# Kernel tuning notes

Measured on AMD Instinct MI355X. Metric: run time of the kernel, lower is better.

The kernel has to match this reference:

```python
import jax, jax.numpy as jnp
import numpy as np

D_MODEL = 1024
N_HEADS = 16
HEAD_DIM = D_MODEL // N_HEADS


def setup_inputs() -> dict:
    key = jax.random.key(0)
    k_x, k_wqkv, k_bqkv, k_wo, k_bo = jax.random.split(key, 5)
    B, T = 2, 2048
    scale = 1.0 / np.sqrt(D_MODEL)
    return {
        "x": jax.random.normal(k_x, (B, T, D_MODEL), dtype=jnp.float32),
        "W_qkv": jax.random.normal(k_wqkv, (D_MODEL, 3 * D_MODEL), dtype=jnp.float32) * scale,
        "b_qkv": jax.random.normal(k_bqkv, (3 * D_MODEL,), dtype=jnp.float32) * 0.01,
        "W_out": jax.random.normal(k_wo, (D_MODEL, D_MODEL), dtype=jnp.float32) * scale,
        "b_out": jax.random.normal(k_bo, (D_MODEL,), dtype=jnp.float32) * 0.01,
    }


def reference(x, W_qkv, b_qkv, W_out, b_out):
    B, T, C = x.shape
    qkv = x @ W_qkv + b_qkv                      # [B,T,3C]
    q, k, v = jnp.split(qkv, 3, axis=-1)
    def heads(t):
        return t.reshape(B, T, N_HEADS, HEAD_DIM).transpose(0, 2, 1, 3)  # [B,H,T,d]
    q, k, v = heads(q), heads(k), heads(v)
    att = jnp.einsum('bhqd,bhkd->bhqk', q, k) / np.sqrt(HEAD_DIM)
    causal = jnp.tril(jnp.ones((T, T), dtype=bool))
    att = jnp.where(causal, att, -jnp.inf)
    att = jax.nn.softmax(att, axis=-1)
    out = jnp.einsum('bhqk,bhkd->bhqd', att, v)  # [B,H,T,d]
    out = out.transpose(0, 2, 1, 3).reshape(B, T, C)
    return out @ W_out + b_out
```

## Files before the change

### kernel.cpp

```cpp
#include <hip/hip_runtime.h>
#include <hip/hip_bf16.h>
#include <math.h>

typedef __bf16 bf16;
typedef __attribute__((ext_vector_type(8))) __bf16 bf16x8;
typedef __attribute__((ext_vector_type(4))) __bf16 bf16x4;
typedef __attribute__((ext_vector_type(4))) short s16x4;
typedef __attribute__((ext_vector_type(4))) float f32x4;

#define T_SEQ 2048

static __device__ __forceinline__ float fast_exp2(float x) {
#if __has_builtin(__builtin_amdgcn_exp2f)
    return __builtin_amdgcn_exp2f(x);
#else
    return __expf(x * 0.69314718f);
#endif
}

static __device__ __forceinline__ void gload_lds16(const bf16* g, bf16* l) {
    __builtin_amdgcn_global_load_lds((const __attribute__((address_space(1))) void*)g,
                                     (__attribute__((address_space(3))) void*)l, 16, 0, 0);
}

static __device__ __forceinline__ int swz(int row, int colb) {
    return row * 128 + (colb ^ ((row & 7) << 4));
}

__global__ void convert_kernel(const float* __restrict__ x, bf16* __restrict__ xb, int n4)
{
    int i = blockIdx.x * blockDim.x + threadIdx.x;
    int stride = gridDim.x * blockDim.x;
    for (; i < n4; i += stride) {
        f32x4 v = ((const f32x4*)x)[i];
        bf16x4 o;
        o[0] = (bf16)v[0]; o[1] = (bf16)v[1]; o[2] = (bf16)v[2]; o[3] = (bf16)v[3];
        ((bf16x4*)xb)[i] = o;
    }
}

__global__ __launch_bounds__(256) void transpose_conv_kernel(
    const float* __restrict__ W, bf16* __restrict__ Wt, int K, int N)
{
    __shared__ float tile[32][33];
    int tx = threadIdx.x & 31, ty = threadIdx.x >> 5;
    int n0 = blockIdx.x * 32, k0 = blockIdx.y * 32;
#pragma unroll
    for (int j = 0; j < 4; ++j)
        tile[ty + j * 8][tx] = W[(size_t)(k0 + ty + j * 8) * N + n0 + tx];
    __syncthreads();
#pragma unroll
    for (int j = 0; j < 4; ++j)
        Wt[(size_t)(n0 + ty + j * 8) * K + k0 + tx] = (bf16)tile[tx][ty + j * 8];
}

__global__ __launch_bounds__(256) void vtrans_kernel(
    const bf16* __restrict__ qkv, bf16* __restrict__ Vt)
{
    __shared__ bf16 tile[64][72];
    const int tid = threadIdx.x;
    const int bh = blockIdx.y, b = bh >> 4, h = bh & 15;
    const int t0 = blockIdx.x * 64;
    const size_t base = (size_t)b * T_SEQ * 3072 + 2048 + h * 64;
    const int r = tid >> 3, c = (tid & 7) * 8;
    *(bf16x8*)&tile[r][c]      = *(const bf16x8*)&qkv[base + (size_t)(t0 + r) * 3072 + c];
    *(bf16x8*)&tile[r + 32][c] = *(const bf16x8*)&qkv[base + (size_t)(t0 + r + 32) * 3072 + c];
    __syncthreads();
    bf16x8 o0, o1;
#pragma unroll
    for (int j = 0; j < 8; ++j) { o0[j] = tile[c + j][r]; o1[j] = tile[c + j][r + 32]; }
    *(bf16x8*)&Vt[((size_t)bh * 64 + r) * T_SEQ + t0 + c] = o0;
    *(bf16x8*)&Vt[((size_t)bh * 64 + r + 32) * T_SEQ + t0 + c] = o1;
}

template<int BM, int BN, int BLK, int WGN, int OUT_BF16>
__global__ __launch_bounds__(BLK, 2) void gemm2ph_kernel(
    const bf16* __restrict__ A, const bf16* __restrict__ Bt,
    const float* __restrict__ bias, void* __restrict__ Cout,
    int M, int N, int K, int GX)
{
    constexpr int WAVES = BLK / 64, WGM = WAVES / WGN;
    constexpr int MR = BM / (WGM * 16), NR = BN / (WGN * 16);
    constexpr int A_RND = BM * 8 / BLK, B_RND = BN * 8 / BLK;
    constexpr int LDS_HALF = (BM + BN) * 128;
    __shared__ __align__(16) char lds[2 * LDS_HALF];

    const int tid = threadIdx.x, lane = tid & 63, wid = tid >> 6;
    const int wm = wid / WGN, wn = wid % WGN;
    const int l15 = lane & 15, l4 = lane >> 4;
    const int cpx = gridDim.x >> 3;
    const int sbid = ((int)blockIdx.x & 7) * cpx + ((int)blockIdx.x >> 3);
    const int m0 = (sbid / GX) * BM, n0 = (sbid % GX) * BN;
    const int wu = tid & ~63;

    f32x4 acc[MR][NR] = {};
    const int NT = K >> 6;

    auto stage = [&](int b, int kt) {
        char* Ab = lds + b * LDS_HALF;
        char* Bb = Ab + BM * 128;
#pragma unroll
        for (int j = 0; j < A_RND; ++j) {
            int ch = j * BLK + tid, r = ch >> 3;
            int c = ((ch & 7) ^ (r & 7)) * 8;
            gload_lds16(&A[(size_t)(m0 + r) * K + kt + c],
                        (bf16*)Ab + (size_t)(j * BLK + wu) * 8);
        }
#pragma unroll
        for (int j = 0; j < B_RND; ++j) {
            int ch = j * BLK + tid, r = ch >> 3;
            int c = ((ch & 7) ^ (r & 7)) * 8;
            gload_lds16(&Bt[(size_t)(n0 + r) * K + kt + c],
                        (bf16*)Bb + (size_t)(j * BLK + wu) * 8);
        }
    };

    stage(0, 0);
    asm volatile("s_waitcnt vmcnt(0)" ::: "memory");
    __builtin_amdgcn_s_barrier();

    for (int t = 0; t < NT; ++t) {
        if (t + 1 < NT) stage((t + 1) & 1, (t + 1) * 64);
        const char* Ab = lds + (t & 1) * LDS_HALF;
        const char* Bb = Ab + BM * 128;
#pragma unroll
        for (int kk = 0; kk < 2; ++kk) {
            bf16x8 af[MR], bfr[NR];
#pragma unroll
            for (int mi = 0; mi < MR; ++mi) {
                int row = wm * (MR * 16) + mi * 16 + l15;
                af[mi] = *(const bf16x8*)(Ab + swz(row, kk * 64 + l4 * 16));
            }
#pragma unroll
            for (int ni = 0; ni < NR; ++ni) {
                int row = wn * (NR * 16) + ni * 16 + l15;
                bfr[ni] = *(const bf16x8*)(Bb + swz(row, kk * 64 + l4 * 16));
            }
#pragma unroll
            for (int mi = 0; mi < MR; ++mi)
#pragma unroll
                for (int ni = 0; ni < NR; ++ni)
                    acc[mi][ni] = __builtin_amdgcn_mfma_f32_16x16x32_bf16(
                        af[mi], bfr[ni], acc[mi][ni], 0, 0, 0);
        }
        asm volatile("s_waitcnt vmcnt(0)" ::: "memory");
        __builtin_amdgcn_s_barrier();
    }

#pragma unroll
    for (int mi = 0; mi < MR; ++mi) {
#pragma unroll
        for (int ni = 0; ni < NR; ++ni) {
            int col = n0 + wn * (NR * 16) + ni * 16 + l15;
            float bv = bias[col];
#pragma unroll
            for (int r = 0; r < 4; ++r) {
                int row = m0 + wm * (MR * 16) + mi * 16 + l4 * 4 + r;
                float v = acc[mi][ni][r] + bv;
                if (OUT_BF16) ((bf16*)Cout)[(size_t)row * N + col] = (bf16)v;
                else          ((float*)Cout)[(size_t)row * N + col] = v;
            }
        }
    }
}

__global__ __launch_bounds__(256, 3) void attn_kernel(
    const bf16* __restrict__ qkv, const bf16* __restrict__ Vt, bf16* __restrict__ attb)
{
    __shared__ __align__(16) char smem[32768];
    const int tid = threadIdx.x, lane = tid & 63, wid = tid >> 6;
    const int qg = wid >> 1, par = wid & 1;
    const int bid = blockIdx.x;
    const int iq = 31 - (bid >> 5);
    const int bh = bid & 31, b = bh >> 4, h = bh & 15;
    const int nt = iq + 1, npairs = (nt + 1) >> 1;
    const int l15 = lane & 15, l4 = lane >> 4;
    const size_t base = (size_t)b * T_SEQ * 3072;
    const int koff = 1024 + h * 64;
    const size_t vtb = (size_t)bh * 64 * T_SEQ;
    const int sr = tid >> 2, sq4 = tid & 3;

    const int q0 = iq * 64 + qg * 32;
    bf16x8 Qf[2][2];
#pragma unroll
    for (int qf = 0; qf < 2; ++qf)
#pragma unroll
        for (int dh = 0; dh < 2; ++dh)
            Qf[qf][dh] = *(const bf16x8*)&qkv[base + (size_t)(q0 + qf * 16 + l15) * 3072
                                             + h * 64 + dh * 32 + l4 * 8];

    f32x4 Oacc[4][2] = {};
    float m_run[2] = { -1e30f, -1e30f };
    float l_run[2] = { 0.f, 0.f };

    bf16x8 kreg[2][2], vreg[2][2];
    {
        const int pb = 0;
#pragma unroll
        for (int p = 0; p < 2; ++p)
#pragma unroll
            for (int j = 0; j < 2; ++j) {
                kreg[p][j] = *(const bf16x8*)&qkv[base + (size_t)(pb + p * 64 + sr) * 3072
                                                 + koff + sq4 * 16 + j * 8];
                vreg[p][j] = *(const bf16x8*)&Vt[vtb + (size_t)sr * T_SEQ + pb + p * 64 + sq4 * 16 + j * 8];
            }
    }

    for (int u = 0; u < npairs; ++u) {
        __syncthreads();
#pragma unroll
        for (int p = 0; p < 2; ++p) {
            char* Kp = smem + p * 8192;
            char* Vp = smem + 16384 + p * 8192;
#pragma unroll
            for (int j = 0; j < 2; ++j) {
                const int byte = swz(sr, sq4 * 32 + j * 16);
                *(bf16x8*)(Kp + byte) = kreg[p][j];
                *(bf16x8*)(Vp + byte) = vreg[p][j];
            }
        }
        __syncthreads();
        if (u + 1 < npairs) {
            const int pb = (u + 1) * 128;
#pragma unroll
            for (int p = 0; p < 2; ++p)
#pragma unroll
                for (int j = 0; j < 2; ++j) {
                    kreg[p][j] = *(const bf16x8*)&qkv[base + (size_t)(pb + p * 64 + sr) * 3072
                                                     + koff + sq4 * 16 + j * 8];
                    vreg[p][j] = *(const bf16x8*)&Vt[vtb + (size_t)sr * T_SEQ + pb + p * 64 + sq4 * 16 + j * 8];
                }
        }
        const int t = 2 * u + par;
        if (t < nt) {
            const char* Kc = smem + par * 8192;
            const char* Vc = smem + 16384 + par * 8192;
            f32x4 S[4][2] = {};
            __builtin_amdgcn_s_setprio(1);
#pragma unroll
            for (int dh = 0; dh < 2; ++dh)
#pragma unroll
                for (int kf = 0; kf < 4; ++kf) {
                    bf16x8 kfr = *(const bf16x8*)(Kc + swz(kf * 16 + l15, dh * 64 + l4 * 16));
#pragma unroll
                    for (int qf = 0; qf < 2; ++qf)
                        S[kf][qf] = __builtin_amdgcn_mfma_f32_16x16x32_bf16(
                            kfr, Qf[qf][dh], S[kf][qf], 0, 0, 0);
                }
            __builtin_amdgcn_s_setprio(0);
            const int diag = (t == nt - 1);
            s16x4 Pb[4][2];
#pragma unroll
            for (int qf = 0; qf < 2; ++qf) {
                float pmax = -3.0e38f;
                if (diag) {
                    const int qq = qg * 32 + qf * 16 + l15;
#pragma unroll
                    for (int kf = 0; kf < 4; ++kf)
#pragma unroll
                        for (int r = 0; r < 4; ++r) {
                            if (kf * 16 + l4 * 4 + r > qq) S[kf][qf][r] = -3.0e38f;
                            pmax = fmaxf(pmax, S[kf][qf][r]);
                        }
                } else {
#pragma unroll
                    for (int kf = 0; kf < 4; ++kf)
#pragma unroll
                        for (int r = 0; r < 4; ++r) pmax = fmaxf(pmax, S[kf][qf][r]);
                }
                pmax = fmaxf(pmax, __shfl_xor(pmax, 16));
                pmax = fmaxf(pmax, __shfl_xor(pmax, 32));
                if (!__all(pmax - m_run[qf] <= 64.f)) {
                    float mnew = fmaxf(m_run[qf], pmax);
                    float alpha = fast_exp2((m_run[qf] - mnew) * 0.18033688f);
                    m_run[qf] = mnew;
                    l_run[qf] *= alpha;
#pragma unroll
                    for (int df = 0; df < 4; ++df) Oacc[df][qf] *= alpha;
                }
                float lsum = 0.f;
#pragma unroll
                for (int kf = 0; kf < 4; ++kf)
#pragma unroll
                    for (int r = 0; r < 4; ++r) {
                        float p = fast_exp2((S[kf][qf][r] - m_run[qf]) * 0.18033688f);
                        lsum += p;
                        Pb[kf][qf][r] = __builtin_bit_cast(short, (bf16)p);
                    }
                lsum += __shfl_xor(lsum, 16);
                lsum += __shfl_xor(lsum, 32);
                l_run[qf] += lsum;
            }
            __builtin_amdgcn_s_setprio(1);
#pragma unroll
            for (int kf = 0; kf < 4; ++kf)
#pragma unroll
                for (int df = 0; df < 4; ++df) {
                    bf16x4 av = *(const bf16x4*)(Vc + swz(df * 16 + l15, kf * 32 + l4 * 8));
                    s16x4 avs = __builtin_bit_cast(s16x4, av);
#pragma unroll
                    for (int qf = 0; qf < 2; ++qf)
                        Oacc[df][qf] = __builtin_amdgcn_mfma_f32_16x16x16bf16_1k(
                            avs, Pb[kf][qf], Oacc[df][qf], 0, 0, 0);
                }
            __builtin_amdgcn_s_setprio(0);
        }
    }

    float* cbuf = (float*)smem;
    __syncthreads();
    if (par == 1) {
        float* p = cbuf + (qg * 64 + lane) * 36;
#pragma unroll
        for (int df = 0; df < 4; ++df)
#pragma unroll
            for (int qf = 0; qf < 2; ++qf)
                *(f32x4*)(p + (df * 2 + qf) * 4) = Oacc[df][qf];
        p[32] = m_run[0]; p[33] = m_run[1]; p[34] = l_run[0]; p[35] = l_run[1];
    }
    __syncthreads();
    if (par == 0) {
        const float* p = cbuf + (qg * 64 + lane) * 36;
#pragma unroll
        for (int qf = 0; qf < 2; ++qf) {
            float m1 = p[32 + qf], l1 = p[34 + qf];
            float m = fmaxf(m_run[qf], m1);
            float a0 = fast_exp2((m_run[qf] - m) * 0.18033688f);
            float a1 = fast_exp2((m1 - m) * 0.18033688f);
            float inv = 1.f / (l_run[qf] * a0 + l1 * a1);
            const int qrow = q0 + qf * 16 + l15;
#pragma unroll
            for (int df = 0; df < 4; ++df) {
                const float* po = p + (df * 2 + qf) * 4;
                bf16x4 o;
#pragma unroll
                for (int r = 0; r < 4; ++r)
                    o[r] = (bf16)((Oacc[df][qf][r] * a0 + po[r] * a1) * inv);
                *(bf16x4*)&attb[((size_t)b * T_SEQ + qrow) * 1024 + h * 64 + df * 16 + l4 * 4] = o;
            }
        }
    }
}

extern "C" void kernel_launch(void* const* d_in, const int* in_sizes, int n_in,
                              void* d_out, int out_size, void* d_ws, size_t ws_size,
                              hipStream_t stream)
{
    const float* x    = (const float*)d_in[0];
    const float* Wqkv = (const float*)d_in[1];
    const float* bqkv = (const float*)d_in[2];
    const float* Wout = (const float*)d_in[3];
    const float* bout = (const float*)d_in[4];
    float* out = (float*)d_out;

    char* ws = (char*)d_ws;
    bf16* xb    = (bf16*)(ws);
    bf16* Vt    = (bf16*)(ws);
    bf16* Wqkvt = (bf16*)(ws + (8ull  << 20));
    bf16* Woutt = (bf16*)(ws + (14ull << 20));
    bf16* qkvb  = (bf16*)(ws + (16ull << 20));
    bf16* attb  = (bf16*)(ws + (40ull << 20));

    convert_kernel<<<dim3(2048), dim3(256), 0, stream>>>(x, xb, (4096 * 1024) / 4);
    transpose_conv_kernel<<<dim3(96, 32), dim3(256), 0, stream>>>(Wqkv, Wqkvt, 1024, 3072);
    transpose_conv_kernel<<<dim3(32, 32), dim3(256), 0, stream>>>(Wout, Woutt, 1024, 1024);
    gemm2ph_kernel<256, 192, 512, 4, 1><<<dim3(256), dim3(512), 0, stream>>>(
        xb, Wqkvt, bqkv, (void*)qkvb, 4096, 3072, 1024, 16);
    vtrans_kernel<<<dim3(32, 32), dim3(256), 0, stream>>>(qkvb, Vt);
    attn_kernel<<<dim3(1024), dim3(256), 0, stream>>>(qkvb, Vt, attb);
    gemm2ph_kernel<128, 128, 256, 2, 0><<<dim3(256), dim3(256), 0, stream>>>(
        attb, Woutt, bout, (void*)out, 4096, 1024, 1024, 8);
}
```

Measured before the change: 105.1 us.

## Switch attention MFMAs to 32x32x16 tiles with permlane32 P repacking

Rewrites the attention inner loops to use 32x32x16 bf16 MFMA instructions instead of 16x16 variants, so each wave holds one 32-row query tile with a single running max and sum. The P matrix is converted from the QK^T output layout to the B-operand layout in registers with permlane32_swap, which avoids LDS round trips and the 16-lane shuffle. This cuts the MFMA instruction count and the number of LDS fragment loads, and simplifies the softmax reductions. The larger accumulators (16 floats each) change register pressure and may affect occupancy under launch_bounds(256,3).

```diff
diff --git a/kernel.cpp b/kernel.cpp
--- a/kernel.cpp
+++ b/kernel.cpp
@@ -7,6 +7,8 @@
 typedef __attribute__((ext_vector_type(4))) __bf16 bf16x4;
 typedef __attribute__((ext_vector_type(4))) short s16x4;
 typedef __attribute__((ext_vector_type(4))) float f32x4;
+typedef __attribute__((ext_vector_type(16))) float f32x16;
+typedef __attribute__((ext_vector_type(4))) unsigned u32x4;
 
 #define T_SEQ 2048
 
@@ -16,6 +18,12 @@
 #else
     return __expf(x * 0.69314718f);
 #endif
+}
+
+static __device__ __forceinline__ unsigned pk(float lo, float hi) {
+    unsigned a = (unsigned)__builtin_bit_cast(unsigned short, (bf16)lo);
+    unsigned b = (unsigned)__builtin_bit_cast(unsigned short, (bf16)hi);
+    return a | (b << 16);
 }
 
 static __device__ __forceinline__ void gload_lds16(const bf16* g, bf16* l) {
@@ -174,35 +182,32 @@
     const int iq = 31 - (bid >> 5);
     const int bh = bid & 31, b = bh >> 4, h = bh & 15;
     const int nt = iq + 1, npairs = (nt + 1) >> 1;
-    const int l15 = lane & 15, l4 = lane >> 4;
+    const int l31 = lane & 31, hi = lane >> 5, hib = hi * 16;
     const size_t base = (size_t)b * T_SEQ * 3072;
     const int koff = 1024 + h * 64;
     const size_t vtb = (size_t)bh * 64 * T_SEQ;
     const int sr = tid >> 2, sq4 = tid & 3;
 
     const int q0 = iq * 64 + qg * 32;
-    bf16x8 Qf[2][2];
-#pragma unroll
-    for (int qf = 0; qf < 2; ++qf)
-#pragma unroll
-        for (int dh = 0; dh < 2; ++dh)
-            Qf[qf][dh] = *(const bf16x8*)&qkv[base + (size_t)(q0 + qf * 16 + l15) * 3072
-                                             + h * 64 + dh * 32 + l4 * 8];
-
-    f32x4 Oacc[4][2] = {};
-    float m_run[2] = { -1e30f, -1e30f };
-    float l_run[2] = { 0.f, 0.f };
+    const int qrow = q0 + l31;
+
+    bf16x8 Qf[4];
+#pragma unroll
+    for (int ds = 0; ds < 4; ++ds)
+        Qf[ds] = *(const bf16x8*)&qkv[base + (size_t)qrow * 3072 + h * 64 + ds * 16 + hi * 8];
+
+    f32x16 Oacc[2] = {};
+    float m_run = -1e30f, l_run = 0.f;
 
     bf16x8 kreg[2][2], vreg[2][2];
     {
-        const int pb = 0;
 #pragma unroll
         for (int p = 0; p < 2; ++p)
 #pragma unroll
             for (int j = 0; j < 2; ++j) {
-                kreg[p][j] = *(const bf16x8*)&qkv[base + (size_t)(pb + p * 64 + sr) * 3072
+                kreg[p][j] = *(const bf16x8*)&qkv[base + (size_t)(p * 64 + sr) * 3072
                                                  + koff + sq4 * 16 + j * 8];
-                vreg[p][j] = *(const bf16x8*)&Vt[vtb + (size_t)sr * T_SEQ + pb + p * 64 + sq4 * 16 + j * 8];
+                vreg[p][j] = *(const bf16x8*)&Vt[vtb + (size_t)sr * T_SEQ + p * 64 + sq4 * 16 + j * 8];
             }
     }
 
@@ -235,74 +240,72 @@
         if (t < nt) {
             const char* Kc = smem + par * 8192;
             const char* Vc = smem + 16384 + par * 8192;
-            f32x4 S[4][2] = {};
+            f32x16 S[2] = {};
             __builtin_amdgcn_s_setprio(1);
 #pragma unroll
-            for (int dh = 0; dh < 2; ++dh)
-#pragma unroll
-                for (int kf = 0; kf < 4; ++kf) {
-                    bf16x8 kfr = *(const bf16x8*)(Kc + swz(kf * 16 + l15, dh * 64 + l4 * 16));
-#pragma unroll
-                    for (int qf = 0; qf < 2; ++qf)
-                        S[kf][qf] = __builtin_amdgcn_mfma_f32_16x16x32_bf16(
-                            kfr, Qf[qf][dh], S[kf][qf], 0, 0, 0);
+            for (int ds = 0; ds < 4; ++ds)
+#pragma unroll
+                for (int kt = 0; kt < 2; ++kt) {
+                    bf16x8 af = *(const bf16x8*)(Kc + swz(kt * 32 + l31, ds * 32 + hib));
+                    S[kt] = __builtin_amdgcn_mfma_f32_32x32x16_bf16(af, Qf[ds], S[kt], 0, 0, 0);
                 }
             __builtin_amdgcn_s_setprio(0);
-            const int diag = (t == nt - 1);
-            s16x4 Pb[4][2];
-#pragma unroll
-            for (int qf = 0; qf < 2; ++qf) {
-                float pmax = -3.0e38f;
-                if (diag) {
-                    const int qq = qg * 32 + qf * 16 + l15;
-#pragma unroll
-                    for (int kf = 0; kf < 4; ++kf)
-#pragma unroll
-                        for (int r = 0; r < 4; ++r) {
-                            if (kf * 16 + l4 * 4 + r > qq) S[kf][qf][r] = -3.0e38f;
-                            pmax = fmaxf(pmax, S[kf][qf][r]);
-                        }
-                } else {
-#pragma unroll
-                    for (int kf = 0; kf < 4; ++kf)
-#pragma unroll
-                        for (int r = 0; r < 4; ++r) pmax = fmaxf(pmax, S[kf][qf][r]);
+            float pmax = -3.0e38f;
+            if (t == nt - 1) {
+                const int qloc = qg * 32 + l31;
+#pragma unroll
+                for (int kt = 0; kt < 2; ++kt)
+#pragma unroll
+                    for (int j = 0; j < 16; ++j) {
+                        const int kloc = kt * 32 + (j & 3) + 8 * (j >> 2) + 4 * hi;
+                        if (kloc > qloc) S[kt][j] = -3.0e38f;
+                        pmax = fmaxf(pmax, S[kt][j]);
+                    }
+            } else {
+#pragma unroll
+                for (int kt = 0; kt < 2; ++kt)
+#pragma unroll
+                    for (int j = 0; j < 16; ++j) pmax = fmaxf(pmax, S[kt][j]);
+            }
+            pmax = fmaxf(pmax, __shfl_xor(pmax, 32));
+            if (!__all(pmax - m_run <= 64.f)) {
+                float mnew = fmaxf(m_run, pmax);
+                float alpha = fast_exp2((m_run - mnew) * 0.18033688f);
+                m_run = mnew;
+                l_run *= alpha;
+                Oacc[0] *= alpha;
+                Oacc[1] *= alpha;
+            }
+            float lsum = 0.f;
+#pragma unroll
+            for (int kt = 0; kt < 2; ++kt)
+#pragma unroll
+                for (int j = 0; j < 16; ++j) {
+                    float p = fast_exp2((S[kt][j] - m_run) * 0.18033688f);
+                    S[kt][j] = p;
+                    lsum += p;
                 }
-                pmax = fmaxf(pmax, __shfl_xor(pmax, 16));
-                pmax = fmaxf(pmax, __shfl_xor(pmax, 32));
-                if (!__all(pmax - m_run[qf] <= 64.f)) {
-                    float mnew = fmaxf(m_run[qf], pmax);
-                    float alpha = fast_exp2((m_run[qf] - mnew) * 0.18033688f);
-                    m_run[qf] = mnew;
-                    l_run[qf] *= alpha;
-#pragma unroll
-                    for (int df = 0; df < 4; ++df) Oacc[df][qf] *= alpha;
+            lsum += __shfl_xor(lsum, 32);
+            l_run += lsum;
+            __builtin_amdgcn_s_setprio(1);
+#pragma unroll
+            for (int ks = 0; ks < 4; ++ks) {
+                const int kt = ks >> 1, bs = (ks & 1) * 8;
+                unsigned P01 = pk(S[kt][bs + 0], S[kt][bs + 1]);
+                unsigned P23 = pk(S[kt][bs + 2], S[kt][bs + 3]);
+                unsigned P45 = pk(S[kt][bs + 4], S[kt][bs + 5]);
+                unsigned P67 = pk(S[kt][bs + 6], S[kt][bs + 7]);
+                auto r02 = __builtin_amdgcn_permlane32_swap(P01, P45, false, false);
+                auto r13 = __builtin_amdgcn_permlane32_swap(P23, P67, false, false);
+                u32x4 wv;
+                wv[0] = r02[0]; wv[1] = r13[0]; wv[2] = r02[1]; wv[3] = r13[1];
+                bf16x8 Bfrag = __builtin_bit_cast(bf16x8, wv);
+#pragma unroll
+                for (int dt = 0; dt < 2; ++dt) {
+                    bf16x8 av = *(const bf16x8*)(Vc + swz(dt * 32 + l31, ks * 32 + hib));
+                    Oacc[dt] = __builtin_amdgcn_mfma_f32_32x32x16_bf16(av, Bfrag, Oacc[dt], 0, 0, 0);
                 }
-                float lsum = 0.f;
-#pragma unroll
-                for (int kf = 0; kf < 4; ++kf)
-#pragma unroll
-                    for (int r = 0; r < 4; ++r) {
-                        float p = fast_exp2((S[kf][qf][r] - m_run[qf]) * 0.18033688f);
-                        lsum += p;
-                        Pb[kf][qf][r] = __builtin_bit_cast(short, (bf16)p);
-                    }
-                lsum += __shfl_xor(lsum, 16);
-                lsum += __shfl_xor(lsum, 32);
-                l_run[qf] += lsum;
-            }
-            __builtin_amdgcn_s_setprio(1);
-#pragma unroll
-            for (int kf = 0; kf < 4; ++kf)
-#pragma unroll
-                for (int df = 0; df < 4; ++df) {
-                    bf16x4 av = *(const bf16x4*)(Vc + swz(df * 16 + l15, kf * 32 + l4 * 8));
-                    s16x4 avs = __builtin_bit_cast(s16x4, av);
-#pragma unroll
-                    for (int qf = 0; qf < 2; ++qf)
-                        Oacc[df][qf] = __builtin_amdgcn_mfma_f32_16x16x16bf16_1k(
-                            avs, Pb[kf][qf], Oacc[df][qf], 0, 0, 0);
-                }
+            }
             __builtin_amdgcn_s_setprio(0);
         }
     }
@@ -312,31 +315,29 @@
     if (par == 1) {
         float* p = cbuf + (qg * 64 + lane) * 36;
 #pragma unroll
-        for (int df = 0; df < 4; ++df)
-#pragma unroll
-            for (int qf = 0; qf < 2; ++qf)
-                *(f32x4*)(p + (df * 2 + qf) * 4) = Oacc[df][qf];
-        p[32] = m_run[0]; p[33] = m_run[1]; p[34] = l_run[0]; p[35] = l_run[1];
+        for (int dt = 0; dt < 2; ++dt)
+#pragma unroll
+            for (int j = 0; j < 16; ++j) p[dt * 16 + j] = Oacc[dt][j];
+        p[32] = m_run; p[33] = l_run;
     }
     __syncthreads();
     if (par == 0) {
         const float* p = cbuf + (qg * 64 + lane) * 36;
-#pragma unroll
-        for (int qf = 0; qf < 2; ++qf) {
-            float m1 = p[32 + qf], l1 = p[34 + qf];
-            float m = fmaxf(m_run[qf], m1);
-            float a0 = fast_exp2((m_run[qf] - m) * 0.18033688f);
-            float a1 = fast_exp2((m1 - m) * 0.18033688f);
-            float inv = 1.f / (l_run[qf] * a0 + l1 * a1);
-            const int qrow = q0 + qf * 16 + l15;
-#pragma unroll
-            for (int df = 0; df < 4; ++df) {
-                const float* po = p + (df * 2 + qf) * 4;
+        float m1 = p[32], l1 = p[33];
+        float m = fmaxf(m_run, m1);
+        float a0 = fast_exp2((m_run - m) * 0.18033688f);
+        float a1 = fast_exp2((m1 - m) * 0.18033688f);
+        float inv = 1.f / (l_run * a0 + l1 * a1);
+#pragma unroll
+        for (int dt = 0; dt < 2; ++dt) {
+#pragma unroll
+            for (int g = 0; g < 4; ++g) {
                 bf16x4 o;
 #pragma unroll
-                for (int r = 0; r < 4; ++r)
-                    o[r] = (bf16)((Oacc[df][qf][r] * a0 + po[r] * a1) * inv);
-                *(bf16x4*)&attb[((size_t)b * T_SEQ + qrow) * 1024 + h * 64 + df * 16 + l4 * 4] = o;
+                for (int j = 0; j < 4; ++j)
+                    o[j] = (bf16)((Oacc[dt][g * 4 + j] * a0 + p[dt * 16 + g * 4 + j] * a1) * inv);
+                const int d = dt * 32 + g * 8 + 4 * hi;
+                *(bf16x4*)&attb[((size_t)b * T_SEQ + qrow) * 1024 + h * 64 + d] = o;
             }
         }
     }
```

New measurement: 101.5 us. 3.4% less time.
